# Performance work log

Measured on AMD Instinct MI355X. Metric: run time of the kernel, lower is better.

Reference implementation:

```python
import jax, jax.numpy as jnp
import numpy as np

D_MODEL = 768
D_INNER = 1536      # expand=2
D_STATE = 16
DT_RANK = 48        # ceil(768/16)
D_CONV = 4
DEPTH = 24
NUM_CLASSES = 527
GRID = (8, 64)      # (128/16, 1024/16)
SEQ = GRID[0] * GRID[1]
TOKPOS = SEQ // 2   # middle cls token position


def setup_inputs() -> dict:
    key = jax.random.key(0)
    ks = jax.random.split(key, 12)
    rn = lambda k, s, sc=0.02: jax.random.normal(k, s, jnp.float32) * sc
    A_init = jnp.log(jnp.arange(1, D_STATE + 1, dtype=jnp.float32))  # S4D-real init
    return {
        "x": jax.random.normal(ks[0], (1, 1, 128, 1024), jnp.float32),
        "patch_w": rn(ks[1], (D_MODEL, 1, 16, 16)),
        "patch_b": jnp.zeros((D_MODEL,), jnp.float32),
        "cls_token": rn(ks[2], (1, 1, D_MODEL)),
        "pos_embed": rn(ks[3], (1, SEQ + 1, D_MODEL)),
        "in_proj_w": rn(ks[4], (DEPTH, 2 * D_INNER, D_MODEL)),
        "conv_w": rn(ks[5], (DEPTH, 2, D_INNER, D_CONV), 0.1),
        "conv_b": jnp.zeros((DEPTH, 2, D_INNER), jnp.float32),
        "xproj_w": rn(ks[6], (DEPTH, 2, DT_RANK + 2 * D_STATE, D_INNER)),
        "dtproj_w": rn(ks[7], (DEPTH, 2, D_INNER, DT_RANK), 0.1),
        "dtproj_b": jnp.full((DEPTH, 2, D_INNER), float(np.log(np.expm1(0.01))), jnp.float32),
        "A_log": jnp.ones((DEPTH, 2, D_INNER, 1), jnp.float32) * A_init,
        "D_skip": jnp.ones((DEPTH, 2, D_INNER), jnp.float32),
        "out_proj_w": rn(ks[8], (DEPTH, D_MODEL, D_INNER)),
        "norm_w": jnp.ones((DEPTH, D_MODEL), jnp.float32),
        "norm_f_w": jnp.ones((D_MODEL,), jnp.float32),
        "head_w": rn(ks[9], (NUM_CLASSES, D_MODEL)),
        "head_b": jnp.zeros((NUM_CLASSES,), jnp.float32),
    }


def _rmsnorm(x, w, eps=1e-5):
    return x * jax.lax.rsqrt(jnp.mean(x * x, axis=-1, keepdims=True) + eps) * w


def _causal_conv_silu(x, w, b):
    # x [B,d,L], depthwise causal conv, kernel D_CONV, left-pad D_CONV-1
    L = x.shape[-1]
    xp = jnp.pad(x, ((0, 0), (0, 0), (D_CONV - 1, 0)))
    y = sum(w[:, k, None] * xp[:, :, k:k + L] for k in range(D_CONV)) + b[:, None]
    return jax.nn.silu(y)


def _selective_scan(dt, A, Bm, C, u):
    # dt,u: [B,d,L]; Bm,C: [B,N,L]; A: [d,N] (negative)
    def step(h, inp):
        dt_t, B_t, C_t, u_t = inp           # [B,d],[B,N],[B,N],[B,d]
        h = h * jnp.exp(dt_t[..., None] * A) + (dt_t * u_t)[..., None] * B_t[:, None, :]
        return h, jnp.einsum('bdn,bn->bd', h, C_t)
    h0 = jnp.zeros((dt.shape[0], A.shape[0], A.shape[1]), dt.dtype)
    mv = lambda a: jnp.moveaxis(a, -1, 0)
    _, ys = jax.lax.scan(step, h0, (mv(dt), mv(Bm), mv(C), mv(u)))
    return jnp.moveaxis(ys, 0, -1)          # [B,d,L]


def _mamba_dir(x, z, cw, cb, xw, dw, db, A_log, Dsk):
    xc = _causal_conv_silu(x, cw, cb)
    dbl = jnp.einsum('bdl,cd->bcl', xc, xw)                 # [B, R+2N, L]
    dt = jax.nn.softplus(jnp.einsum('brl,dr->bdl', dbl[:, :DT_RANK], dw) + db[:, None])
    Bm = dbl[:, DT_RANK:DT_RANK + D_STATE]
    C = dbl[:, DT_RANK + D_STATE:]
    y = _selective_scan(dt, -jnp.exp(A_log), Bm, C, xc) + Dsk[:, None] * xc
    return y * jax.nn.silu(z)


def _block(carry, p):
    hidden, residual = carry
    ipw, cw, cb, xw, dw, db, A_log, Dsk, opw, nw = p
    residual = residual + hidden                            # add -> norm -> mixer
    h = _rmsnorm(residual, nw)
    xz = jnp.einsum('bld,ed->ble', h, ipw)                  # [B,L,2*d_inner]
    x, z = jnp.split(jnp.moveaxis(xz, -1, 1), 2, axis=1)    # each [B,d_inner,L]
    yf = _mamba_dir(x, z, cw[0], cb[0], xw[0], dw[0], db[0], A_log[0], Dsk[0])
    yb = _mamba_dir(x[:, :, ::-1], z[:, :, ::-1], cw[1], cb[1], xw[1], dw[1],
                    db[1], A_log[1], Dsk[1])[:, :, ::-1]
    out = jnp.einsum('bdl,ed->ble', (yf + yb) * 0.5, opw)   # if_devide_out
    return (out, residual), None


def reference(x, patch_w, patch_b, cls_token, pos_embed, in_proj_w, conv_w, conv_b,
              xproj_w, dtproj_w, dtproj_b, A_log, D_skip, out_proj_w, norm_w,
              norm_f_w, head_w, head_b):
    h = jax.lax.conv_general_dilated(x, patch_w, (16, 16), 'VALID',
                                     dimension_numbers=('NCHW', 'OIHW', 'NCHW'))
    h = h + patch_b[None, :, None, None]
    B = h.shape[0]
    h = h.reshape(B, D_MODEL, SEQ).transpose(0, 2, 1)       # [B,512,768]
    cls = jnp.broadcast_to(cls_token, (B, 1, D_MODEL))
    h = jnp.concatenate([h[:, :TOKPOS], cls, h[:, TOKPOS:]], axis=1)  # [B,513,768]
    h = h + pos_embed
    carry = (h, jnp.zeros_like(h))
    (hidden, residual), _ = jax.lax.scan(
        _block, carry,
        (in_proj_w, conv_w, conv_b, xproj_w, dtproj_w, dtproj_b, A_log, D_skip,
         out_proj_w, norm_w))
    out = _rmsnorm(residual + hidden, norm_f_w)
    feat = out[:, TOKPOS]                                   # middle cls token
    return feat @ head_w.T + head_b
```

## Files before the change

kernel.cpp:

```cpp
#include <hip/hip_runtime.h>

#define L_SEQ 513
#define DM 768
#define DI 1536
#define DSTATE 16
#define DTRANK 48
#define NCLS 527
#define DEPTH 24
#define NC 32
#define CLEN 17
#define SKI 3
#define SKX 8
#define SKO 8

typedef unsigned short u16;
typedef __bf16 bf16x8 __attribute__((ext_vector_type(8)));
typedef float f32x4 __attribute__((ext_vector_type(4)));

#define MFMA_BF16(A, B, C) __builtin_amdgcn_mfma_f32_16x16x32_bf16(A, B, C, 0, 0, 0)

__device__ inline u16 f2bf(float x) {
  unsigned u = __float_as_uint(x);
  return (u16)((u + 0x7FFFu + ((u >> 16) & 1u)) >> 16);
}
__device__ inline float bf2f(u16 h) { return __uint_as_float((unsigned)h << 16); }
__device__ inline void split2(float v, u16& h, u16& l) {
  h = f2bf(v);
  l = f2bf(v - bf2f(h));
}
__device__ __forceinline__ int lofs(int row, int g) {
  int swz = (row & 3) ^ ((row >> 2) & 3);
  return row * 32 + ((g ^ swz) << 3);
}

__global__ void wconvert_kernel(const float* __restrict__ src,
                                u16* __restrict__ hi, u16* __restrict__ lo,
                                long n4) {
  long i = (long)blockIdx.x * 256 + threadIdx.x;
  long stride = (long)gridDim.x * 256;
  for (; i < n4; i += stride) {
    float4 v = ((const float4*)src)[i];
    ushort4 h, l;
    split2(v.x, h.x, l.x);
    split2(v.y, h.y, l.y);
    split2(v.z, h.z, l.z);
    split2(v.w, h.w, l.w);
    ((ushort4*)hi)[i] = h;
    ((ushort4*)lo)[i] = l;
  }
}

__global__ void patch_embed_kernel(const float* __restrict__ x,
                                   const float* __restrict__ pw,
                                   const float* __restrict__ pb,
                                   const float* __restrict__ cls,
                                   const float* __restrict__ pos,
                                   float* __restrict__ hidden,
                                   float* __restrict__ residual) {
  int c = blockIdx.x * 256 + threadIdx.x;
  int s = blockIdx.y;
  if (c >= DM) return;
  float val;
  if (s == 256) {
    val = cls[c];
  } else {
    int p = s - (s > 256 ? 1 : 0);
    int gy = p >> 6, gx = p & 63;
    const float* xp = x + gy * 16 * 1024 + gx * 16;
    const float* wp = pw + c * 256;
    float acc = pb[c];
#pragma unroll 4
    for (int ky = 0; ky < 16; ++ky)
#pragma unroll
      for (int kx = 0; kx < 16; ++kx)
        acc += xp[ky * 1024 + kx] * wp[ky * 16 + kx];
    val = acc;
  }
  long idx = (long)s * DM + c;
  hidden[idx] = val + pos[idx];
  residual[idx] = 0.f;
}

__global__ void rmsnorm_kernel(const float* __restrict__ hp, int nparts, long pstr,
                               float* __restrict__ residual,
                               u16* __restrict__ hnh, u16* __restrict__ hnl,
                               const float* __restrict__ w) {
  int t = blockIdx.x;
  float* rrow = residual + (long)t * DM;
  int tid = threadIdx.x;
  float vals[3];
  float ss = 0.f;
#pragma unroll
  for (int i = 0; i < 3; ++i) {
    int c = tid + i * 256;
    float v = rrow[c];
    for (int p = 0; p < nparts; ++p) v += hp[(long)p * pstr + (long)t * DM + c];
    vals[i] = v;
    rrow[c] = v;
    ss += v * v;
  }
#pragma unroll
  for (int o = 32; o; o >>= 1) ss += __shfl_down(ss, o, 64);
  __shared__ float sacc[4];
  if ((tid & 63) == 0) sacc[tid >> 6] = ss;
  __syncthreads();
  float tot = sacc[0] + sacc[1] + sacc[2] + sacc[3];
  float rs = rsqrtf(tot / (float)DM + 1e-5f);
#pragma unroll
  for (int i = 0; i < 3; ++i) {
    int c = tid + i * 256;
    float y = vals[i] * rs * w[c];
    u16 h, l;
    split2(y, h, l);
    hnh[(long)t * DM + c] = h;
    hnl[(long)t * DM + c] = l;
  }
}

#define LOADSTEP(KB)                                                    \
  {                                                                     \
    int k_ = (KB) + g0 * 8;                                             \
    bool kk_ = (k_ + 8 <= kend);                                        \
    uint4 zz = {0, 0, 0, 0};                                            \
    a0h = (kk_ && am0) ? *(const uint4*)(Ahb + aoff0 + k_) : zz;        \
    a1h = (kk_ && am1) ? *(const uint4*)(Ahb + aoff1 + k_) : zz;        \
    a0l = (kk_ && am0) ? *(const uint4*)(Alb + aoff0 + k_) : zz;        \
    a1l = (kk_ && am1) ? *(const uint4*)(Alb + aoff1 + k_) : zz;        \
    b0h = (kk_ && bm0) ? *(const uint4*)(Bhb + boff0 + k_) : zz;        \
    b1h = (kk_ && bm1) ? *(const uint4*)(Bhb + boff1 + k_) : zz;        \
    b0l = (kk_ && bm0) ? *(const uint4*)(Blb + boff0 + k_) : zz;        \
    b1l = (kk_ && bm1) ? *(const uint4*)(Blb + boff1 + k_) : zz;        \
  }
#define WRITEBUF(B)                        \
  {                                        \
    *(uint4*)&SA[B][0][l0] = a0h;          \
    *(uint4*)&SA[B][0][l1] = a1h;          \
    *(uint4*)&SA[B][1][l0] = a0l;          \
    *(uint4*)&SA[B][1][l1] = a1l;          \
    *(uint4*)&SB[B][0][l0] = b0h;          \
    *(uint4*)&SB[B][0][l1] = b1h;          \
    *(uint4*)&SB[B][1][l0] = b0l;          \
    *(uint4*)&SB[B][1][l1] = b1l;          \
  }

__global__ __launch_bounds__(256) void gemm128(
    const u16* __restrict__ Ah, const u16* __restrict__ Al,
    const u16* __restrict__ Bh, const u16* __restrict__ Bl,
    float* __restrict__ C,
    int M, int N, int K, int lda, int ldb, int ldc,
    long sA, long sB, long sC,
    int NSK, int Kb, long sP,
    const float* __restrict__ bias, long sBias, int act) {
  int z = blockIdx.z;
  int batch = z / NSK, sk = z - batch * NSK;
  const u16* Ahb = Ah + (long)batch * sA;
  const u16* Alb = Al + (long)batch * sA;
  const u16* Bhb = Bh + (long)batch * sB;
  const u16* Blb = Bl + (long)batch * sB;
  float* Cb = C + (long)batch * sC + (long)sk * sP;
  const float* biasb = bias ? bias + (long)batch * sBias : nullptr;
  int ks0 = sk * Kb;
  int kend = min(ks0 + Kb, K);

  __shared__ u16 SA[2][2][128 * 32];
  __shared__ u16 SB[2][2][128 * 32];

  int tid = threadIdx.x;
  int m0 = blockIdx.y * 128, n0 = blockIdx.x * 128;

  int r0 = tid >> 2, g0 = tid & 3;
  int r1 = r0 + 64;
  int l0 = lofs(r0, g0), l1 = lofs(r1, g0);
  long aoff0 = (long)(m0 + r0) * lda, aoff1 = (long)(m0 + r1) * lda;
  long boff0 = (long)(n0 + r0) * ldb, boff1 = (long)(n0 + r1) * ldb;
  bool am0 = (m0 + r0) < M, am1 = (m0 + r1) < M;
  bool bm0 = (n0 + r0) < N, bm1 = (n0 + r1) < N;

  int lane = tid & 63, w = tid >> 6;
  int wr = w >> 1, wc = w & 1;
  int fr = lane & 15, kh = lane >> 4;
  int offA[4], offB[4];
#pragma unroll
  for (int i = 0; i < 4; ++i) {
    offA[i] = lofs(wr * 64 + i * 16 + fr, kh);
    offB[i] = lofs(wc * 64 + i * 16 + fr, kh);
  }

  f32x4 acc[4][4] = {};
  int nst = (kend - ks0 + 31) >> 5;
  uint4 a0h, a1h, a0l, a1l, b0h, b1h, b0l, b1l;
  LOADSTEP(ks0);
  WRITEBUF(0);
  if (nst > 1) LOADSTEP(ks0 + 32);
  __syncthreads();

  for (int s = 0; s < nst; ++s) {
    int b = s & 1;
    bf16x8 fah[4], fal[4], fbh[4], fbl[4];
#pragma unroll
    for (int i = 0; i < 4; ++i) {
      fah[i] = __builtin_bit_cast(bf16x8, *(const uint4*)&SA[b][0][offA[i]]);
      fal[i] = __builtin_bit_cast(bf16x8, *(const uint4*)&SA[b][1][offA[i]]);
      fbh[i] = __builtin_bit_cast(bf16x8, *(const uint4*)&SB[b][0][offB[i]]);
      fbl[i] = __builtin_bit_cast(bf16x8, *(const uint4*)&SB[b][1][offB[i]]);
    }
#pragma unroll
    for (int mi = 0; mi < 4; ++mi)
#pragma unroll
      for (int ni = 0; ni < 4; ++ni) {
        acc[mi][ni] = MFMA_BF16(fah[mi], fbh[ni], acc[mi][ni]);
        acc[mi][ni] = MFMA_BF16(fah[mi], fbl[ni], acc[mi][ni]);
        acc[mi][ni] = MFMA_BF16(fal[mi], fbh[ni], acc[mi][ni]);
      }
    if (s + 1 < nst) {
      WRITEBUF(b ^ 1);
      if (s + 2 < nst) LOADSTEP(ks0 + (s + 2) * 32);
    }
    __syncthreads();
  }

#pragma unroll
  for (int mi = 0; mi < 4; ++mi)
#pragma unroll
    for (int ni = 0; ni < 4; ++ni) {
      int n = n0 + wc * 64 + ni * 16 + fr;
      if (n >= N) continue;
      float bv = biasb ? biasb[n] : 0.f;
#pragma unroll
      for (int r = 0; r < 4; ++r) {
        int m = m0 + wr * 64 + mi * 16 + kh * 4 + r;
        if (m >= M) continue;
        float v = acc[mi][ni][r] + bv;
        if (act == 1) v = (v > 20.f) ? v : log1pf(__expf(v));
        Cb[(long)m * ldc + n] = v;
      }
    }
}

__global__ void conv_silu_kernel(const float* __restrict__ xz_p,
                                 const float* __restrict__ cw,
                                 const float* __restrict__ cb,
                                 float* __restrict__ xc,
                                 u16* __restrict__ xch, u16* __restrict__ xcl) {
  const long PZ = (long)L_SEQ * 2 * DI;
  int dir = blockIdx.y;
  int idx = blockIdx.x * 256 + threadIdx.x;
  int d = idx % DI;
  int t = idx / DI;
  const float* w = cw + ((long)dir * DI + d) * 4;
  float acc = cb[dir * DI + d];
#pragma unroll
  for (int k = 0; k < 4; ++k) {
    int tau = t + k - 3;
    if (tau >= 0) {
      int tsrc = dir ? (L_SEQ - 1 - tau) : tau;
      long o = (long)tsrc * (2 * DI) + d;
      float xv = xz_p[o] + xz_p[o + PZ] + xz_p[o + 2 * PZ];
      acc += w[k] * xv;
    }
  }
  float s = acc / (1.f + __expf(-acc));
  long o = ((long)dir * L_SEQ + t) * DI + d;
  xc[o] = s;
  u16 h, l;
  split2(s, h, l);
  xch[o] = h;
  xcl[o] = l;
}

__global__ void xreduce_kernel(const float* __restrict__ dbl_p,
                               float* __restrict__ dbl,
                               u16* __restrict__ d48h, u16* __restrict__ d48l) {
  int idx = blockIdx.x * 256 + threadIdx.x;
  if (idx >= 2 * L_SEQ * 80) return;
  int j = idx % 80;
  int td = idx / 80;
  int dir = td / L_SEQ;
  int t = td - dir * L_SEQ;
  const float* p = dbl_p + (long)dir * SKX * L_SEQ * 80 + (long)t * 80 + j;
  float v = 0.f;
#pragma unroll
  for (int q = 0; q < SKX; ++q) v += p[(long)q * L_SEQ * 80];
  dbl[((long)dir * L_SEQ + t) * 80 + j] = v;
  if (j < DTRANK) {
    u16 h, l;
    split2(v, h, l);
    long o = ((long)dir * L_SEQ + t) * DTRANK + j;
    d48h[o] = h;
    d48l[o] = l;
  }
}

__global__ __launch_bounds__(256) void scan_all(
    const float* __restrict__ dtv_arr,
    const float* __restrict__ xc,
    const float* __restrict__ dbl,
    const float* __restrict__ xz_p,
    const float* __restrict__ A_log,
    const float* __restrict__ Dsk,
    float* __restrict__ y) {
  const long PZ = (long)L_SEQ * 2 * DI;
  int dir = blockIdx.y;
  int d0 = blockIdx.x * 8;
  int tid = threadIdx.x;
  __shared__ float Q[8][NC][DSTATE];
  __shared__ float Sv[8][NC];

  const float* dtp = dtv_arr + (long)dir * L_SEQ * DI;
  const float* xcp = xc + (long)dir * L_SEQ * DI;
  const float* dblp = dbl + (long)dir * L_SEQ * 80;

  int dl = tid & 7, c = tid >> 3;
  int d = d0 + dl;
  float negA[DSTATE];
#pragma unroll
  for (int n = 0; n < DSTATE; ++n)
    negA[n] = -__expf(A_log[((long)dir * DI + d) * DSTATE + n]);

  int t0 = c * CLEN, t1 = min(t0 + CLEN, L_SEQ);
  {
    float h[DSTATE];
#pragma unroll
    for (int n = 0; n < DSTATE; ++n) h[n] = 0.f;
    float S = 0.f;
    for (int t = t0; t < t1; ++t) {
      float dt = dtp[(long)t * DI + d];
      float u = xcp[(long)t * DI + d];
      float du = dt * u;
      S += dt;
      const float4* B4 = (const float4*)(dblp + (long)t * 80 + DTRANK);
      float4 b0 = B4[0], b1 = B4[1], b2 = B4[2], b3 = B4[3];
      float Bv[DSTATE] = {b0.x, b0.y, b0.z, b0.w, b1.x, b1.y, b1.z, b1.w,
                          b2.x, b2.y, b2.z, b2.w, b3.x, b3.y, b3.z, b3.w};
#pragma unroll
      for (int n = 0; n < DSTATE; ++n)
        h[n] = h[n] * __expf(dt * negA[n]) + du * Bv[n];
    }
    Sv[dl][c] = S;
#pragma unroll
    for (int n = 0; n < DSTATE; ++n) Q[dl][c][n] = h[n];
  }
  __syncthreads();
  if (tid < 128) {
    int fdl = tid >> 4, n = tid & 15;
    int fd = d0 + fdl;
    float nA = -__expf(A_log[((long)dir * DI + fd) * DSTATE + n]);
    float h = 0.f;
    for (int cc = 0; cc < NC; ++cc) {
      float S = Sv[fdl][cc];
      float q = Q[fdl][cc][n];
      Q[fdl][cc][n] = h;
      h = h * __expf(nA * S) + q;
    }
  }
  __syncthreads();
  {
    float h[DSTATE];
#pragma unroll
    for (int n = 0; n < DSTATE; ++n) h[n] = Q[dl][c][n];
    float dskip = Dsk[dir * DI + d];
    for (int t = t0; t < t1; ++t) {
      float dt = dtp[(long)t * DI + d];
      float u = xcp[(long)t * DI + d];
      float du = dt * u;
      const float4* B4 = (const float4*)(dblp + (long)t * 80 + DTRANK);
      float4 b0 = B4[0], b1 = B4[1], b2 = B4[2], b3 = B4[3];
      float4 c0 = B4[4], c1 = B4[5], c2 = B4[6], c3 = B4[7];
      float Bv[DSTATE] = {b0.x, b0.y, b0.z, b0.w, b1.x, b1.y, b1.z, b1.w,
                          b2.x, b2.y, b2.z, b2.w, b3.x, b3.y, b3.z, b3.w};
      float Cv[DSTATE] = {c0.x, c0.y, c0.z, c0.w, c1.x, c1.y, c1.z, c1.w,
                          c2.x, c2.y, c2.z, c2.w, c3.x, c3.y, c3.z, c3.w};
      float acc = 0.f;
#pragma unroll
      for (int n = 0; n < DSTATE; ++n) {
        h[n] = h[n] * __expf(dt * negA[n]) + du * Bv[n];
        acc += h[n] * Cv[n];
      }
      int tsrc = dir ? (L_SEQ - 1 - t) : t;
      long zo = (long)tsrc * (2 * DI) + DI + d;
      float zv = xz_p[zo] + xz_p[zo + PZ] + xz_p[zo + 2 * PZ];
      float sz = zv / (1.f + __expf(-zv));
      y[((long)dir * L_SEQ + tsrc) * DI + d] = (acc + dskip * u) * sz;
    }
  }
}

__global__ void yavg_kernel(const float* __restrict__ yf,
                            const float* __restrict__ yb,
                            u16* __restrict__ yh, u16* __restrict__ yl) {
  long i = (long)blockIdx.x * 256 + threadIdx.x;
  if (i >= (long)L_SEQ * DI / 4) return;
  float4 a = ((const float4*)yf)[i];
  float4 b = ((const float4*)yb)[i];
  ushort4 h, l;
  split2(0.5f * (a.x + b.x), h.x, l.x);
  split2(0.5f * (a.y + b.y), h.y, l.y);
  split2(0.5f * (a.z + b.z), h.z, l.z);
  split2(0.5f * (a.w + b.w), h.w, l.w);
  ((ushort4*)yh)[i] = h;
  ((ushort4*)yl)[i] = l;
}

__global__ void head_kernel(const float* __restrict__ residual,
                            const float* __restrict__ hp, long pstr,
                            const float* __restrict__ nfw,
                            const float* __restrict__ hw,
                            const float* __restrict__ hb,
                            float* __restrict__ out) {
  int j = blockIdx.x;
  int tid = threadIdx.x;
  const float* r = residual + (long)256 * DM;
  float ss = 0.f, dp = 0.f;
#pragma unroll
  for (int i = 0; i < 3; ++i) {
    int c = tid + i * 256;
    float v = r[c];
    for (int p = 0; p < SKO; ++p) v += hp[(long)p * pstr + (long)256 * DM + c];
    ss += v * v;
    dp += v * nfw[c] * hw[(long)j * DM + c];
  }
#pragma unroll
  for (int o = 32; o; o >>= 1) {
    ss += __shfl_down(ss, o, 64);
    dp += __shfl_down(dp, o, 64);
  }
  __shared__ float s1[4], s2[4];
  if ((tid & 63) == 0) {
    s1[tid >> 6] = ss;
    s2[tid >> 6] = dp;
  }
  __syncthreads();
  if (tid == 0) {
    float tot = s1[0] + s1[1] + s1[2] + s1[3];
    float d = s2[0] + s2[1] + s2[2] + s2[3];
    out[j] = d * rsqrtf(tot / (float)DM + 1e-5f) + hb[j];
  }
}

extern "C" void kernel_launch(void* const* d_in, const int* in_sizes, int n_in,
                              void* d_out, int out_size, void* d_ws, size_t ws_size,
                              hipStream_t stream) {
  const float* x        = (const float*)d_in[0];
  const float* patch_w  = (const float*)d_in[1];
  const float* patch_b  = (const float*)d_in[2];
  const float* cls_tok  = (const float*)d_in[3];
  const float* pos_emb  = (const float*)d_in[4];
  const float* in_proj  = (const float*)d_in[5];
  const float* conv_w   = (const float*)d_in[6];
  const float* conv_b   = (const float*)d_in[7];
  const float* xproj_w  = (const float*)d_in[8];
  const float* dtproj_w = (const float*)d_in[9];
  const float* dtproj_b = (const float*)d_in[10];
  const float* A_log    = (const float*)d_in[11];
  const float* D_skip   = (const float*)d_in[12];
  const float* out_proj = (const float*)d_in[13];
  const float* norm_w   = (const float*)d_in[14];
  const float* norm_f_w = (const float*)d_in[15];
  const float* head_w   = (const float*)d_in[16];
  const float* head_b   = (const float*)d_in[17];
  float* out = (float*)d_out;

  const long PHN = (long)L_SEQ * DM;
  const long PZ  = (long)L_SEQ * 2 * DI;

  float* ws = (float*)d_ws;
  float* residual = ws; ws += PHN;
  float* xz_p     = ws; ws += SKI * PZ;
  float* xc       = ws; ws += (long)2 * L_SEQ * DI;
  float* dbl      = ws; ws += (long)2 * L_SEQ * 80;
  float* dbl_p    = ws; ws += (long)2 * SKX * L_SEQ * 80;
  float* dtb      = ws; ws += (long)2 * L_SEQ * DI;
  float* yb       = ws; ws += (long)2 * L_SEQ * DI;
  float* hid_p    = ws; ws += (long)SKO * PHN;

  u16* wsu = (u16*)ws;
  const long N_HN  = PHN;
  const long N_XC  = (long)2 * L_SEQ * DI;
  const long N_D48 = (long)2 * L_SEQ * DTRANK;
  const long N_YA  = (long)L_SEQ * DI;
  const long N_WI  = (long)DEPTH * 2 * DI * DM;
  const long N_WX  = (long)DEPTH * 2 * 80 * DI;
  const long N_WD  = (long)DEPTH * 2 * DI * DTRANK;
  const long N_WO  = (long)DEPTH * DM * DI;
  u16* hn_h  = wsu; wsu += N_HN;
  u16* hn_l  = wsu; wsu += N_HN;
  u16* xc_h  = wsu; wsu += N_XC;
  u16* xc_l  = wsu; wsu += N_XC;
  u16* d48_h = wsu; wsu += N_D48;
  u16* d48_l = wsu; wsu += N_D48;
  u16* ya_h  = wsu; wsu += N_YA;
  u16* ya_l  = wsu; wsu += N_YA;
  u16* wi_h  = wsu; wsu += N_WI;
  u16* wi_l  = wsu; wsu += N_WI;
  u16* wx_h  = wsu; wsu += N_WX;
  u16* wx_l  = wsu; wsu += N_WX;
  u16* wd_h  = wsu; wsu += N_WD;
  u16* wd_l  = wsu; wsu += N_WD;
  u16* wo_h  = wsu; wsu += N_WO;
  u16* wo_l  = wsu; wsu += N_WO;

  wconvert_kernel<<<2048, 256, 0, stream>>>(in_proj,  wi_h, wi_l, N_WI / 4);
  wconvert_kernel<<<512,  256, 0, stream>>>(xproj_w,  wx_h, wx_l, N_WX / 4);
  wconvert_kernel<<<512,  256, 0, stream>>>(dtproj_w, wd_h, wd_l, N_WD / 4);
  wconvert_kernel<<<2048, 256, 0, stream>>>(out_proj, wo_h, wo_l, N_WO / 4);

  patch_embed_kernel<<<dim3(3, L_SEQ), 256, 0, stream>>>(
      x, patch_w, patch_b, cls_tok, pos_emb, hid_p, residual);

  for (int l = 0; l < DEPTH; ++l) {
    const u16* wih = wi_h + (long)l * 2 * DI * DM;
    const u16* wil = wi_l + (long)l * 2 * DI * DM;
    const u16* wxh = wx_h + (long)l * 2 * 80 * DI;
    const u16* wxl = wx_l + (long)l * 2 * 80 * DI;
    const u16* wdh = wd_h + (long)l * 2 * DI * DTRANK;
    const u16* wdl = wd_l + (long)l * 2 * DI * DTRANK;
    const u16* woh = wo_h + (long)l * DM * DI;
    const u16* wol = wo_l + (long)l * DM * DI;
    const float* cw  = conv_w   + (long)l * 2 * DI * 4;
    const float* cb  = conv_b   + (long)l * 2 * DI;
    const float* db  = dtproj_b + (long)l * 2 * DI;
    const float* Al  = A_log    + (long)l * 2 * DI * DSTATE;
    const float* Dk  = D_skip   + (long)l * 2 * DI;
    const float* nw  = norm_w   + (long)l * DM;

    rmsnorm_kernel<<<L_SEQ, 256, 0, stream>>>(
        hid_p, (l == 0) ? 1 : SKO, PHN, residual, hn_h, hn_l, nw);

    gemm128<<<dim3(24, 5, SKI), 256, 0, stream>>>(
        hn_h, hn_l, wih, wil, xz_p, L_SEQ, 2 * DI, DM, DM, DM, 2 * DI,
        0, 0, 0, SKI, DM / SKI, PZ, nullptr, 0, 0);

    conv_silu_kernel<<<dim3(3078, 2), 256, 0, stream>>>(xz_p, cw, cb, xc, xc_h, xc_l);

    gemm128<<<dim3(1, 5, 2 * SKX), 256, 0, stream>>>(
        xc_h, xc_l, wxh, wxl, dbl_p, L_SEQ, 80, DI, DI, DI, 80,
        (long)L_SEQ * DI, (long)80 * DI, (long)SKX * L_SEQ * 80,
        SKX, DI / SKX, (long)L_SEQ * 80, nullptr, 0, 0);

    xreduce_kernel<<<(2 * L_SEQ * 80 + 255) / 256, 256, 0, stream>>>(
        dbl_p, dbl, d48_h, d48_l);

    gemm128<<<dim3(12, 5, 2), 256, 0, stream>>>(
        d48_h, d48_l, wdh, wdl, dtb, L_SEQ, DI, DTRANK, DTRANK, DTRANK, DI,
        (long)L_SEQ * DTRANK, (long)DI * DTRANK, (long)L_SEQ * DI,
        1, DTRANK, 0, db, DI, 1);

    scan_all<<<dim3(DI / 8, 2), 256, 0, stream>>>(
        dtb, xc, dbl, xz_p, Al, Dk, yb);

    yavg_kernel<<<(L_SEQ * DI / 4 + 255) / 256, 256, 0, stream>>>(
        yb, yb + (long)L_SEQ * DI, ya_h, ya_l);

    gemm128<<<dim3(6, 5, SKO), 256, 0, stream>>>(
        ya_h, ya_l, woh, wol, hid_p, L_SEQ, DM, DI, DI, DI, DM,
        0, 0, 0, SKO, DI / SKO, PHN, nullptr, 0, 0);
  }

  head_kernel<<<NCLS, 256, 0, stream>>>(residual, hid_p, PHN,
                                        norm_f_w, head_w, head_b, out);
}
```

Measured before the change: 4.010 ms.

## Fuse dt projection into scan, yavg into out_proj GEMM, drop x_proj split-K

The dt_proj GEMM plus softplus moves inside the selective scan, which recomputes the 48-term dot product per timestep from the per-channel weights held in registers. The forward/backward averaging and bf16 split now happen in the out_proj GEMM's A-load path, a new template mode that reads fp32. The x_proj GEMM drops split-K so it writes dbl directly, which removes the reduce kernel. The conv+SiLU kernel is vectorised to process four channels per thread. This removes three kernel launches and their intermediate buffers per layer, at the cost of redundant dot products in the scan (run twice, once per pass) and an x_proj GEMM with only 10 blocks.

```diff
diff --git a/kernel.cpp b/kernel.cpp
--- a/kernel.cpp
+++ b/kernel.cpp
@@ -10,7 +10,6 @@
 #define NC 32
 #define CLEN 17
 #define SKI 3
-#define SKX 8
 #define SKO 8
 
 typedef unsigned short u16;
@@ -117,48 +116,29 @@
   }
 }
 
-#define LOADSTEP(KB)                                                    \
-  {                                                                     \
-    int k_ = (KB) + g0 * 8;                                             \
-    bool kk_ = (k_ + 8 <= kend);                                        \
-    uint4 zz = {0, 0, 0, 0};                                            \
-    a0h = (kk_ && am0) ? *(const uint4*)(Ahb + aoff0 + k_) : zz;        \
-    a1h = (kk_ && am1) ? *(const uint4*)(Ahb + aoff1 + k_) : zz;        \
-    a0l = (kk_ && am0) ? *(const uint4*)(Alb + aoff0 + k_) : zz;        \
-    a1l = (kk_ && am1) ? *(const uint4*)(Alb + aoff1 + k_) : zz;        \
-    b0h = (kk_ && bm0) ? *(const uint4*)(Bhb + boff0 + k_) : zz;        \
-    b1h = (kk_ && bm1) ? *(const uint4*)(Bhb + boff1 + k_) : zz;        \
-    b0l = (kk_ && bm0) ? *(const uint4*)(Blb + boff0 + k_) : zz;        \
-    b1l = (kk_ && bm1) ? *(const uint4*)(Blb + boff1 + k_) : zz;        \
-  }
-#define WRITEBUF(B)                        \
-  {                                        \
-    *(uint4*)&SA[B][0][l0] = a0h;          \
-    *(uint4*)&SA[B][0][l1] = a1h;          \
-    *(uint4*)&SA[B][1][l0] = a0l;          \
-    *(uint4*)&SA[B][1][l1] = a1l;          \
-    *(uint4*)&SB[B][0][l0] = b0h;          \
-    *(uint4*)&SB[B][0][l1] = b1h;          \
-    *(uint4*)&SB[B][1][l0] = b0l;          \
-    *(uint4*)&SB[B][1][l1] = b1l;          \
-  }
-
+template <int AMODE>
 __global__ __launch_bounds__(256) void gemm128(
-    const u16* __restrict__ Ah, const u16* __restrict__ Al,
+    const void* __restrict__ A0, const void* __restrict__ A1,
     const u16* __restrict__ Bh, const u16* __restrict__ Bl,
     float* __restrict__ C,
     int M, int N, int K, int lda, int ldb, int ldc,
-    long sA, long sB, long sC,
-    int NSK, int Kb, long sP,
-    const float* __restrict__ bias, long sBias, int act) {
+    long sA, long sB, long sC, int NSK, int Kb, long sP) {
   int z = blockIdx.z;
   int batch = z / NSK, sk = z - batch * NSK;
-  const u16* Ahb = Ah + (long)batch * sA;
-  const u16* Alb = Al + (long)batch * sA;
+  const u16* Ahb = nullptr;
+  const u16* Alb = nullptr;
+  const float* Af = nullptr;
+  const float* Ag = nullptr;
+  if (AMODE == 0) {
+    Ahb = (const u16*)A0 + (long)batch * sA;
+    Alb = (const u16*)A1 + (long)batch * sA;
+  } else {
+    Af = (const float*)A0 + (long)batch * sA;
+    Ag = (const float*)A1 + (long)batch * sA;
+  }
   const u16* Bhb = Bh + (long)batch * sB;
   const u16* Blb = Bl + (long)batch * sB;
   float* Cb = C + (long)batch * sC + (long)sk * sP;
-  const float* biasb = bias ? bias + (long)batch * sBias : nullptr;
   int ks0 = sk * Kb;
   int kend = min(ks0 + Kb, K);
 
@@ -186,12 +166,58 @@
     offB[i] = lofs(wc * 64 + i * 16 + fr, kh);
   }
 
+  uint4 a0h, a1h, a0l, a1l, b0h, b1h, b0l, b1l;
+  auto loadA = [&](long rowoff, bool ok, int k_, uint4& hh, uint4& ll) {
+    uint4 z4 = {0, 0, 0, 0};
+    if (AMODE == 0) {
+      hh = ok ? *(const uint4*)(Ahb + rowoff + k_) : z4;
+      ll = ok ? *(const uint4*)(Alb + rowoff + k_) : z4;
+    } else {
+      if (!ok) { hh = z4; ll = z4; return; }
+      float4 f0 = *(const float4*)(Af + rowoff + k_);
+      float4 f1 = *(const float4*)(Af + rowoff + k_ + 4);
+      float4 g0v = *(const float4*)(Ag + rowoff + k_);
+      float4 g1v = *(const float4*)(Ag + rowoff + k_ + 4);
+      u16 ha[8], la[8];
+      split2(0.5f * (f0.x + g0v.x), ha[0], la[0]);
+      split2(0.5f * (f0.y + g0v.y), ha[1], la[1]);
+      split2(0.5f * (f0.z + g0v.z), ha[2], la[2]);
+      split2(0.5f * (f0.w + g0v.w), ha[3], la[3]);
+      split2(0.5f * (f1.x + g1v.x), ha[4], la[4]);
+      split2(0.5f * (f1.y + g1v.y), ha[5], la[5]);
+      split2(0.5f * (f1.z + g1v.z), ha[6], la[6]);
+      split2(0.5f * (f1.w + g1v.w), ha[7], la[7]);
+      hh = *(const uint4*)ha;
+      ll = *(const uint4*)la;
+    }
+  };
+  auto loadstep = [&](int kb) {
+    int k_ = kb + g0 * 8;
+    bool kk = (k_ + 8 <= kend);
+    uint4 z4 = {0, 0, 0, 0};
+    loadA(aoff0, kk && am0, k_, a0h, a0l);
+    loadA(aoff1, kk && am1, k_, a1h, a1l);
+    b0h = (kk && bm0) ? *(const uint4*)(Bhb + boff0 + k_) : z4;
+    b1h = (kk && bm1) ? *(const uint4*)(Bhb + boff1 + k_) : z4;
+    b0l = (kk && bm0) ? *(const uint4*)(Blb + boff0 + k_) : z4;
+    b1l = (kk && bm1) ? *(const uint4*)(Blb + boff1 + k_) : z4;
+  };
+  auto writebuf = [&](int b) {
+    *(uint4*)&SA[b][0][l0] = a0h;
+    *(uint4*)&SA[b][0][l1] = a1h;
+    *(uint4*)&SA[b][1][l0] = a0l;
+    *(uint4*)&SA[b][1][l1] = a1l;
+    *(uint4*)&SB[b][0][l0] = b0h;
+    *(uint4*)&SB[b][0][l1] = b1h;
+    *(uint4*)&SB[b][1][l0] = b0l;
+    *(uint4*)&SB[b][1][l1] = b1l;
+  };
+
   f32x4 acc[4][4] = {};
   int nst = (kend - ks0 + 31) >> 5;
-  uint4 a0h, a1h, a0l, a1l, b0h, b1h, b0l, b1l;
-  LOADSTEP(ks0);
-  WRITEBUF(0);
-  if (nst > 1) LOADSTEP(ks0 + 32);
+  loadstep(ks0);
+  writebuf(0);
+  if (nst > 1) loadstep(ks0 + 32);
   __syncthreads();
 
   for (int s = 0; s < nst; ++s) {
@@ -213,8 +239,8 @@
         acc[mi][ni] = MFMA_BF16(fal[mi], fbh[ni], acc[mi][ni]);
       }
     if (s + 1 < nst) {
-      WRITEBUF(b ^ 1);
-      if (s + 2 < nst) LOADSTEP(ks0 + (s + 2) * 32);
+      writebuf(b ^ 1);
+      if (s + 2 < nst) loadstep(ks0 + (s + 2) * 32);
     }
     __syncthreads();
   }
@@ -225,14 +251,11 @@
     for (int ni = 0; ni < 4; ++ni) {
       int n = n0 + wc * 64 + ni * 16 + fr;
       if (n >= N) continue;
-      float bv = biasb ? biasb[n] : 0.f;
 #pragma unroll
       for (int r = 0; r < 4; ++r) {
         int m = m0 + wr * 64 + mi * 16 + kh * 4 + r;
         if (m >= M) continue;
-        float v = acc[mi][ni][r] + bv;
-        if (act == 1) v = (v > 20.f) ? v : log1pf(__expf(v));
-        Cb[(long)m * ldc + n] = v;
+        Cb[(long)m * ldc + n] = acc[mi][ni][r];
       }
     }
 }
@@ -245,57 +268,55 @@
   const long PZ = (long)L_SEQ * 2 * DI;
   int dir = blockIdx.y;
   int idx = blockIdx.x * 256 + threadIdx.x;
-  int d = idx % DI;
-  int t = idx / DI;
-  const float* w = cw + ((long)dir * DI + d) * 4;
-  float acc = cb[dir * DI + d];
+  if (idx >= L_SEQ * (DI / 4)) return;
+  int d4 = idx % (DI / 4);
+  int t = idx / (DI / 4);
+  int d = d4 * 4;
+  float wv[4][4];
+#pragma unroll
+  for (int j = 0; j < 4; ++j) {
+    float4 wr = *(const float4*)(cw + ((long)dir * DI + d + j) * 4);
+    wv[j][0] = wr.x; wv[j][1] = wr.y; wv[j][2] = wr.z; wv[j][3] = wr.w;
+  }
+  float4 bv = *(const float4*)(cb + (long)dir * DI + d);
+  float a0 = bv.x, a1 = bv.y, a2 = bv.z, a3 = bv.w;
 #pragma unroll
   for (int k = 0; k < 4; ++k) {
     int tau = t + k - 3;
     if (tau >= 0) {
       int tsrc = dir ? (L_SEQ - 1 - tau) : tau;
       long o = (long)tsrc * (2 * DI) + d;
-      float xv = xz_p[o] + xz_p[o + PZ] + xz_p[o + 2 * PZ];
-      acc += w[k] * xv;
-    }
-  }
-  float s = acc / (1.f + __expf(-acc));
+      float4 x0 = *(const float4*)(xz_p + o);
+      float4 x1 = *(const float4*)(xz_p + o + PZ);
+      float4 x2 = *(const float4*)(xz_p + o + 2 * PZ);
+      a0 += wv[0][k] * (x0.x + x1.x + x2.x);
+      a1 += wv[1][k] * (x0.y + x1.y + x2.y);
+      a2 += wv[2][k] * (x0.z + x1.z + x2.z);
+      a3 += wv[3][k] * (x0.w + x1.w + x2.w);
+    }
+  }
+  float4 sv;
+  sv.x = a0 / (1.f + __expf(-a0));
+  sv.y = a1 / (1.f + __expf(-a1));
+  sv.z = a2 / (1.f + __expf(-a2));
+  sv.w = a3 / (1.f + __expf(-a3));
   long o = ((long)dir * L_SEQ + t) * DI + d;
-  xc[o] = s;
-  u16 h, l;
-  split2(s, h, l);
-  xch[o] = h;
-  xcl[o] = l;
-}
-
-__global__ void xreduce_kernel(const float* __restrict__ dbl_p,
-                               float* __restrict__ dbl,
-                               u16* __restrict__ d48h, u16* __restrict__ d48l) {
-  int idx = blockIdx.x * 256 + threadIdx.x;
-  if (idx >= 2 * L_SEQ * 80) return;
-  int j = idx % 80;
-  int td = idx / 80;
-  int dir = td / L_SEQ;
-  int t = td - dir * L_SEQ;
-  const float* p = dbl_p + (long)dir * SKX * L_SEQ * 80 + (long)t * 80 + j;
-  float v = 0.f;
-#pragma unroll
-  for (int q = 0; q < SKX; ++q) v += p[(long)q * L_SEQ * 80];
-  dbl[((long)dir * L_SEQ + t) * 80 + j] = v;
-  if (j < DTRANK) {
-    u16 h, l;
-    split2(v, h, l);
-    long o = ((long)dir * L_SEQ + t) * DTRANK + j;
-    d48h[o] = h;
-    d48l[o] = l;
-  }
+  *(float4*)(xc + o) = sv;
+  ushort4 h, l;
+  split2(sv.x, h.x, l.x);
+  split2(sv.y, h.y, l.y);
+  split2(sv.z, h.z, l.z);
+  split2(sv.w, h.w, l.w);
+  *(ushort4*)(xch + o) = h;
+  *(ushort4*)(xcl + o) = l;
 }
 
 __global__ __launch_bounds__(256) void scan_all(
-    const float* __restrict__ dtv_arr,
     const float* __restrict__ xc,
     const float* __restrict__ dbl,
     const float* __restrict__ xz_p,
+    const float* __restrict__ dtw,
+    const float* __restrict__ dtb,
     const float* __restrict__ A_log,
     const float* __restrict__ Dsk,
     float* __restrict__ y) {
@@ -306,7 +327,6 @@
   __shared__ float Q[8][NC][DSTATE];
   __shared__ float Sv[8][NC];
 
-  const float* dtp = dtv_arr + (long)dir * L_SEQ * DI;
   const float* xcp = xc + (long)dir * L_SEQ * DI;
   const float* dblp = dbl + (long)dir * L_SEQ * 80;
 
@@ -316,20 +336,34 @@
 #pragma unroll
   for (int n = 0; n < DSTATE; ++n)
     negA[n] = -__expf(A_log[((long)dir * DI + d) * DSTATE + n]);
+  float4 dwr[12];
+  {
+    const float4* dwp = (const float4*)(dtw + ((long)dir * DI + d) * DTRANK);
+#pragma unroll
+    for (int q = 0; q < 12; ++q) dwr[q] = dwp[q];
+  }
+  float db_ = dtb[(long)dir * DI + d];
 
   int t0 = c * CLEN, t1 = min(t0 + CLEN, L_SEQ);
+
   {
     float h[DSTATE];
 #pragma unroll
     for (int n = 0; n < DSTATE; ++n) h[n] = 0.f;
     float S = 0.f;
     for (int t = t0; t < t1; ++t) {
-      float dt = dtp[(long)t * DI + d];
+      const float4* R = (const float4*)(dblp + (long)t * 80);
+      float dot = db_;
+#pragma unroll
+      for (int q = 0; q < 12; ++q) {
+        float4 r4 = R[q];
+        dot += r4.x * dwr[q].x + r4.y * dwr[q].y + r4.z * dwr[q].z + r4.w * dwr[q].w;
+      }
+      float dt = (dot > 20.f) ? dot : log1pf(__expf(dot));
       float u = xcp[(long)t * DI + d];
       float du = dt * u;
       S += dt;
-      const float4* B4 = (const float4*)(dblp + (long)t * 80 + DTRANK);
-      float4 b0 = B4[0], b1 = B4[1], b2 = B4[2], b3 = B4[3];
+      float4 b0 = R[12], b1 = R[13], b2 = R[14], b3 = R[15];
       float Bv[DSTATE] = {b0.x, b0.y, b0.z, b0.w, b1.x, b1.y, b1.z, b1.w,
                           b2.x, b2.y, b2.z, b2.w, b3.x, b3.y, b3.z, b3.w};
 #pragma unroll
@@ -358,14 +392,20 @@
     float h[DSTATE];
 #pragma unroll
     for (int n = 0; n < DSTATE; ++n) h[n] = Q[dl][c][n];
-    float dskip = Dsk[dir * DI + d];
+    float dskip = Dsk[(long)dir * DI + d];
     for (int t = t0; t < t1; ++t) {
-      float dt = dtp[(long)t * DI + d];
+      const float4* R = (const float4*)(dblp + (long)t * 80);
+      float dot = db_;
+#pragma unroll
+      for (int q = 0; q < 12; ++q) {
+        float4 r4 = R[q];
+        dot += r4.x * dwr[q].x + r4.y * dwr[q].y + r4.z * dwr[q].z + r4.w * dwr[q].w;
+      }
+      float dt = (dot > 20.f) ? dot : log1pf(__expf(dot));
       float u = xcp[(long)t * DI + d];
       float du = dt * u;
-      const float4* B4 = (const float4*)(dblp + (long)t * 80 + DTRANK);
-      float4 b0 = B4[0], b1 = B4[1], b2 = B4[2], b3 = B4[3];
-      float4 c0 = B4[4], c1 = B4[5], c2 = B4[6], c3 = B4[7];
+      float4 b0 = R[12], b1 = R[13], b2 = R[14], b3 = R[15];
+      float4 c0 = R[16], c1 = R[17], c2 = R[18], c3 = R[19];
       float Bv[DSTATE] = {b0.x, b0.y, b0.z, b0.w, b1.x, b1.y, b1.z, b1.w,
                           b2.x, b2.y, b2.z, b2.w, b3.x, b3.y, b3.z, b3.w};
       float Cv[DSTATE] = {c0.x, c0.y, c0.z, c0.w, c1.x, c1.y, c1.z, c1.w,
@@ -383,22 +423,6 @@
       y[((long)dir * L_SEQ + tsrc) * DI + d] = (acc + dskip * u) * sz;
     }
   }
-}
-
-__global__ void yavg_kernel(const float* __restrict__ yf,
-                            const float* __restrict__ yb,
-                            u16* __restrict__ yh, u16* __restrict__ yl) {
-  long i = (long)blockIdx.x * 256 + threadIdx.x;
-  if (i >= (long)L_SEQ * DI / 4) return;
-  float4 a = ((const float4*)yf)[i];
-  float4 b = ((const float4*)yb)[i];
-  ushort4 h, l;
-  split2(0.5f * (a.x + b.x), h.x, l.x);
-  split2(0.5f * (a.y + b.y), h.y, l.y);
-  split2(0.5f * (a.z + b.z), h.z, l.z);
-  split2(0.5f * (a.w + b.w), h.w, l.w);
-  ((ushort4*)yh)[i] = h;
-  ((ushort4*)yl)[i] = l;
 }
 
 __global__ void head_kernel(const float* __restrict__ residual,
@@ -468,40 +492,28 @@
   float* xz_p     = ws; ws += SKI * PZ;
   float* xc       = ws; ws += (long)2 * L_SEQ * DI;
   float* dbl      = ws; ws += (long)2 * L_SEQ * 80;
-  float* dbl_p    = ws; ws += (long)2 * SKX * L_SEQ * 80;
-  float* dtb      = ws; ws += (long)2 * L_SEQ * DI;
   float* yb       = ws; ws += (long)2 * L_SEQ * DI;
   float* hid_p    = ws; ws += (long)SKO * PHN;
 
   u16* wsu = (u16*)ws;
-  const long N_HN  = PHN;
-  const long N_XC  = (long)2 * L_SEQ * DI;
-  const long N_D48 = (long)2 * L_SEQ * DTRANK;
-  const long N_YA  = (long)L_SEQ * DI;
-  const long N_WI  = (long)DEPTH * 2 * DI * DM;
-  const long N_WX  = (long)DEPTH * 2 * 80 * DI;
-  const long N_WD  = (long)DEPTH * 2 * DI * DTRANK;
-  const long N_WO  = (long)DEPTH * DM * DI;
-  u16* hn_h  = wsu; wsu += N_HN;
-  u16* hn_l  = wsu; wsu += N_HN;
-  u16* xc_h  = wsu; wsu += N_XC;
-  u16* xc_l  = wsu; wsu += N_XC;
-  u16* d48_h = wsu; wsu += N_D48;
-  u16* d48_l = wsu; wsu += N_D48;
-  u16* ya_h  = wsu; wsu += N_YA;
-  u16* ya_l  = wsu; wsu += N_YA;
-  u16* wi_h  = wsu; wsu += N_WI;
-  u16* wi_l  = wsu; wsu += N_WI;
-  u16* wx_h  = wsu; wsu += N_WX;
-  u16* wx_l  = wsu; wsu += N_WX;
-  u16* wd_h  = wsu; wsu += N_WD;
-  u16* wd_l  = wsu; wsu += N_WD;
-  u16* wo_h  = wsu; wsu += N_WO;
-  u16* wo_l  = wsu; wsu += N_WO;
+  const long N_HN = PHN;
+  const long N_XC = (long)2 * L_SEQ * DI;
+  const long N_WI = (long)DEPTH * 2 * DI * DM;
+  const long N_WX = (long)DEPTH * 2 * 80 * DI;
+  const long N_WO = (long)DEPTH * DM * DI;
+  u16* hn_h = wsu; wsu += N_HN;
+  u16* hn_l = wsu; wsu += N_HN;
+  u16* xc_h = wsu; wsu += N_XC;
+  u16* xc_l = wsu; wsu += N_XC;
+  u16* wi_h = wsu; wsu += N_WI;
+  u16* wi_l = wsu; wsu += N_WI;
+  u16* wx_h = wsu; wsu += N_WX;
+  u16* wx_l = wsu; wsu += N_WX;
+  u16* wo_h = wsu; wsu += N_WO;
+  u16* wo_l = wsu; wsu += N_WO;
 
   wconvert_kernel<<<2048, 256, 0, stream>>>(in_proj,  wi_h, wi_l, N_WI / 4);
   wconvert_kernel<<<512,  256, 0, stream>>>(xproj_w,  wx_h, wx_l, N_WX / 4);
-  wconvert_kernel<<<512,  256, 0, stream>>>(dtproj_w, wd_h, wd_l, N_WD / 4);
   wconvert_kernel<<<2048, 256, 0, stream>>>(out_proj, wo_h, wo_l, N_WO / 4);
 
   patch_embed_kernel<<<dim3(3, L_SEQ), 256, 0, stream>>>(
@@ -512,12 +524,11 @@
     const u16* wil = wi_l + (long)l * 2 * DI * DM;
     const u16* wxh = wx_h + (long)l * 2 * 80 * DI;
     const u16* wxl = wx_l + (long)l * 2 * 80 * DI;
-    const u16* wdh = wd_h + (long)l * 2 * DI * DTRANK;
-    const u16* wdl = wd_l + (long)l * 2 * DI * DTRANK;
     const u16* woh = wo_h + (long)l * DM * DI;
     const u16* wol = wo_l + (long)l * DM * DI;
     const float* cw  = conv_w   + (long)l * 2 * DI * 4;
     const float* cb  = conv_b   + (long)l * 2 * DI;
+    const float* dw  = dtproj_w + (long)l * 2 * DI * DTRANK;
     const float* db  = dtproj_b + (long)l * 2 * DI;
     const float* Al  = A_log    + (long)l * 2 * DI * DSTATE;
     const float* Dk  = D_skip   + (long)l * 2 * DI;
@@ -526,34 +537,22 @@
     rmsnorm_kernel<<<L_SEQ, 256, 0, stream>>>(
         hid_p, (l == 0) ? 1 : SKO, PHN, residual, hn_h, hn_l, nw);
 
-    gemm128<<<dim3(24, 5, SKI), 256, 0, stream>>>(
+    gemm128<0><<<dim3(24, 5, SKI), 256, 0, stream>>>(
         hn_h, hn_l, wih, wil, xz_p, L_SEQ, 2 * DI, DM, DM, DM, 2 * DI,
-        0, 0, 0, SKI, DM / SKI, PZ, nullptr, 0, 0);
-
-    conv_silu_kernel<<<dim3(3078, 2), 256, 0, stream>>>(xz_p, cw, cb, xc, xc_h, xc_l);
-
-    gemm128<<<dim3(1, 5, 2 * SKX), 256, 0, stream>>>(
-        xc_h, xc_l, wxh, wxl, dbl_p, L_SEQ, 80, DI, DI, DI, 80,
-        (long)L_SEQ * DI, (long)80 * DI, (long)SKX * L_SEQ * 80,
-        SKX, DI / SKX, (long)L_SEQ * 80, nullptr, 0, 0);
-
-    xreduce_kernel<<<(2 * L_SEQ * 80 + 255) / 256, 256, 0, stream>>>(
-        dbl_p, dbl, d48_h, d48_l);
-
-    gemm128<<<dim3(12, 5, 2), 256, 0, stream>>>(
-        d48_h, d48_l, wdh, wdl, dtb, L_SEQ, DI, DTRANK, DTRANK, DTRANK, DI,
-        (long)L_SEQ * DTRANK, (long)DI * DTRANK, (long)L_SEQ * DI,
-        1, DTRANK, 0, db, DI, 1);
+        0, 0, 0, SKI, DM / SKI, PZ);
+
+    conv_silu_kernel<<<dim3(770, 2), 256, 0, stream>>>(xz_p, cw, cb, xc, xc_h, xc_l);
+
+    gemm128<0><<<dim3(1, 5, 2), 256, 0, stream>>>(
+        xc_h, xc_l, wxh, wxl, dbl, L_SEQ, 80, DI, DI, DI, 80,
+        (long)L_SEQ * DI, (long)80 * DI, (long)L_SEQ * 80, 1, DI, 0);
 
     scan_all<<<dim3(DI / 8, 2), 256, 0, stream>>>(
-        dtb, xc, dbl, xz_p, Al, Dk, yb);
-
-    yavg_kernel<<<(L_SEQ * DI / 4 + 255) / 256, 256, 0, stream>>>(
-        yb, yb + (long)L_SEQ * DI, ya_h, ya_l);
-
-    gemm128<<<dim3(6, 5, SKO), 256, 0, stream>>>(
-        ya_h, ya_l, woh, wol, hid_p, L_SEQ, DM, DI, DI, DI, DM,
-        0, 0, 0, SKO, DI / SKO, PHN, nullptr, 0, 0);
+        xc, dbl, xz_p, dw, db, Al, Dk, yb);
+
+    gemm128<1><<<dim3(6, 5, SKO), 256, 0, stream>>>(
+        yb, yb + (long)L_SEQ * DI, woh, wol, hid_p, L_SEQ, DM, DI, DI, DI, DM,
+        0, 0, 0, SKO, DI / SKO, PHN);
   }
 
   head_kernel<<<NCLS, 256, 0, stream>>>(residual, hid_p, PHN,
```

After: 4.750 ms. 1.18x slower.
